# Optimization experiments

Hardware: AMD Instinct MI355X
Metric: run time of the kernel (lower is better)

The kernel has to match this reference:

```python
import jax, jax.numpy as jnp
import numpy as np

ALPHA = 0.9  # init alpha, adj='DAD'


def setup_inputs() -> dict:
    key = jax.random.key(0)
    k1, k2, k3, k4 = jax.random.split(key, 4)
    N, C, E = 100000, 64, 3200000
    labels = jax.random.uniform(k1, (N, C), dtype=jnp.float32)
    mask = jax.random.randint(k2, (N,), 0, 2).astype(bool)
    src = jax.random.randint(k3, (E,), 0, N, dtype=jnp.int64)
    dst = jax.random.randint(k4, (E,), 0, N, dtype=jnp.int64)
    return {"labels": labels, "mask": mask, "src": src, "dst": dst, "num_layers": 10}


def reference(labels, mask, src, dst, num_layers):
    N = labels.shape[0]
    # mask: y = zeros; y[mask] = labels[mask]
    y0 = jnp.where(mask[:, None], labels, jnp.zeros((), labels.dtype))
    last = (1.0 - ALPHA) * y0  # confidence = 1
    # in-degrees via scatter-count at dst, clamped to >= 1
    degs = jax.ops.segment_sum(jnp.ones(dst.shape, labels.dtype), dst, num_segments=N)
    degs = jnp.maximum(degs, 1.0)
    norm = (degs ** -0.5)[:, None]  # DAD: D^-1/2 on both sides

    def step(y, _):
        y = norm * y                                   # left D^-1/2
        h = jax.ops.segment_sum(y[src], dst, num_segments=N)  # A @ y (copy_u + sum)
        y = ALPHA * h * norm                           # right D^-1/2
        y = jnp.clip(last + y, 0.0, 1.0)               # post_step clamp
        return y, None

    y, _ = jax.lax.scan(step, y0, None, length=num_layers)
    return y
```

## Files before the change

kernel.cpp:

```cpp
#include <hip/hip_runtime.h>
#include <hip/hip_fp16.h>


#define ALPHA 0.9f
#define C 64
#define BSHIFT 7
#define MAXB 1024
#define NCHUNK 256

typedef float f32x4 __attribute__((ext_vector_type(4)));
typedef unsigned int u32;
typedef unsigned int u32x2 __attribute__((ext_vector_type(2)));


__global__ void chunk_hist_kernel(const int* __restrict__ dst, int* __restrict__ cnt,
                                  int E, int epc) {
    __shared__ int h[MAXB];
    for (int i = threadIdx.x; i < MAXB; i += 256) h[i] = 0;
    __syncthreads();
    int c = blockIdx.x;
    int e1 = min(c * epc + epc, E);
    for (int e = c * epc + threadIdx.x; e < e1; e += 256) {
        int d = __builtin_nontemporal_load(&dst[e]);
        atomicAdd(&h[d >> BSHIFT], 1);
    }
    __syncthreads();
    for (int i = threadIdx.x; i < MAXB; i += 256) cnt[i * NCHUNK + c] = h[i];
}

__global__ void chunk_scan_kernel(int* __restrict__ cnt, int* __restrict__ bucket_tot) {
    __shared__ int v[256];
    int b = blockIdx.x;
    int t = threadIdx.x;
    int x = cnt[b * NCHUNK + t];
    v[t] = x;
    __syncthreads();
    for (int off = 1; off < 256; off <<= 1) {
        int add = (t >= off) ? v[t - off] : 0;
        __syncthreads();
        v[t] += add;
        __syncthreads();
    }
    cnt[b * NCHUNK + t] = v[t] - x;
    if (t == 255) bucket_tot[b] = v[255];
}

__global__ void base_scan_kernel(const int* __restrict__ bucket_tot,
                                 int* __restrict__ bucket_base,
                                 int* __restrict__ row_ptr, int N, int E, int nb) {
    __shared__ int v[MAXB];
    int t = threadIdx.x;
    int x = (t < nb) ? bucket_tot[t] : 0;
    v[t] = x;
    __syncthreads();
    for (int off = 1; off < MAXB; off <<= 1) {
        int add = (t >= off) ? v[t - off] : 0;
        __syncthreads();
        v[t] += add;
        __syncthreads();
    }
    bucket_base[t] = v[t] - x;
    if (t == MAXB - 1) { bucket_base[MAXB] = v[MAXB - 1]; row_ptr[N] = E; }
}

__global__ void bucket_scatter_kernel(const int* __restrict__ src, const int* __restrict__ dst,
                                      const int* __restrict__ cnt,
                                      const int* __restrict__ bucket_base,
                                      unsigned* __restrict__ tmp, int E, int epc) {
    __shared__ int cur[MAXB];
    int c = blockIdx.x;
    for (int i = threadIdx.x; i < MAXB; i += 256)
        cur[i] = bucket_base[i] + cnt[i * NCHUNK + c];
    __syncthreads();
    int e1 = min(c * epc + epc, E);
    for (int e = c * epc + threadIdx.x; e < e1; e += 256) {
        int d = __builtin_nontemporal_load(&dst[e]);
        int s = __builtin_nontemporal_load(&src[e]);
        int pos = atomicAdd(&cur[d >> BSHIFT], 1);
        tmp[pos] = ((unsigned)(d & 127) << 24) | (unsigned)s;
    }
}

__global__ void bucket_sort_kernel(const unsigned* __restrict__ tmp,
                                   const int* __restrict__ bucket_base,
                                   int* __restrict__ row_ptr,
                                   float* __restrict__ norm,
                                   int* __restrict__ col, int N) {
    __shared__ int ldeg[128];
    __shared__ int lexc[128];
    __shared__ int lcur[128];
    int b = blockIdx.x;
    int lo = b << BSHIFT;
    int nn = min(128, N - lo);
    int ebeg = bucket_base[b];
    int eend = bucket_base[b + 1];
    int t = threadIdx.x;
    if (t < 128) ldeg[t] = 0;
    __syncthreads();
    for (int e = ebeg + t; e < eend; e += 256) {
        atomicAdd(&ldeg[tmp[e] >> 24], 1);
    }
    __syncthreads();
    if (t < 128) lexc[t] = ldeg[t];
    __syncthreads();
    for (int off = 1; off < 128; off <<= 1) {
        int add = (t >= off && t < 128) ? lexc[t - off] : 0;
        __syncthreads();
        if (t < 128) lexc[t] += add;
        __syncthreads();
    }
    if (t < nn) {
        int rp = ebeg + lexc[t] - ldeg[t];
        row_ptr[lo + t] = rp;
        lcur[t] = rp;
        norm[lo + t] = rsqrtf(fmaxf((float)ldeg[t], 1.0f));
    }
    __syncthreads();
    for (int e = ebeg + t; e < eend; e += 256) {
        unsigned pk = tmp[e];
        int pos = atomicAdd(&lcur[pk >> 24], 1);
        col[pos] = (int)(pk & 0xFFFFFFu);
    }
}

__global__ void pack_col_kernel(int* __restrict__ col, const float* __restrict__ norm,
                                int E) {
    int i = blockIdx.x * blockDim.x + threadIdx.x;
    if (i >= E) return;
    u32 s = (u32)col[i];
    u32 nq = (u32)(norm[s] * 32767.0f + 0.5f);
    col[i] = (int)(s | (nq << 17));
}


__global__ void init_z8_kernel(const float* __restrict__ labels,
                               const int* __restrict__ mask,
                               unsigned char* __restrict__ z8,
                               unsigned char* __restrict__ last8,
                               int total8 ) {
    int i = blockIdx.x * blockDim.x + threadIdx.x;
    if (i >= total8) return;
    int node = i >> 3;
    int g = i & 7;
    const float* lrow = labels + (size_t)node * C + g * 8;
    f32x4 a  = __builtin_nontemporal_load((const f32x4*)lrow);
    f32x4 bv = __builtin_nontemporal_load((const f32x4*)lrow + 1);
    bool mk = mask[node] != 0;
    float v[8] = {a.x, a.y, a.z, a.w, bv.x, bv.y, bv.z, bv.w};
    float m = mk ? 255.0f : 0.0f;
    u32 q0 = 0, q1 = 0;
#pragma unroll
    for (int k = 0; k < 4; ++k) q0 |= ((u32)(v[k] * m + 0.5f)) << (8 * k);
#pragma unroll
    for (int k = 0; k < 4; ++k) q1 |= ((u32)(v[k + 4] * m + 0.5f)) << (8 * k);
    u32x2 qq; qq.x = q0; qq.y = q1;
    ((u32x2*)(z8 + (size_t)node * C))[g] = qq;
    ((u32x2*)(last8 + (size_t)node * C))[g] = qq;
}


template <bool OUT_FP32>
__global__ void prop_kernel(const unsigned char* __restrict__ z8_old,
                            unsigned char* __restrict__ z8_new,
                            void* __restrict__ out_f32,
                            const int* __restrict__ row_ptr,
                            const int* __restrict__ col,
                            const float* __restrict__ norm,
                            const unsigned char* __restrict__ last8, int N) {
    int gtid = blockIdx.x * blockDim.x + threadIdx.x;
    int wid = gtid >> 6;
    int lane = threadIdx.x & 63;
    int node = (wid << 1) + (lane >> 5);
    int sub = (lane >> 3) & 3;
    int ch8 = lane & 7;

    bool ok = node < N;
    int beg = 0, end = 0;
    if (ok) { beg = row_ptr[node]; end = row_ptr[node + 1]; }
    int deg = end - beg;
    int lastc = max(end - 1, 0);
    int Tl = (deg + 3) >> 2;
    int T = max(Tl, __shfl_xor(Tl, 32, 64));

    const float DQ = 1.0f / (32767.0f * 255.0f);

    float acc[8];
#pragma unroll
    for (int k = 0; k < 8; ++k) acc[k] = 0.0f;

    if (T > 0) {
        int base = beg + sub;

        float n0, n1, n2, n3, n4, n5, n6, n7;
        uint2 r0, r1, r2, r3, r4, r5, r6, r7;

#define FETCH(t, nv, rv)                                                      \
        do {                                                                  \
            int pp = base + ((t) << 2);                                       \
            int pcl = min(pp, lastc);                                         \
            u32 pk = (u32)col[pcl];                                           \
            int sv = (int)(pk & 0x1FFFFu);                                    \
            float sc = (float)(pk >> 17) * DQ;                                \
            nv = (pp < end) ? sc : 0.0f;                                      \
            rv = ((const uint2*)(z8_old + (size_t)sv * C))[ch8];              \
        } while (0)

#define CONSUME(nv, rv)                                                       \
        do {                                                                  \
            u32 q0 = rv.x, q1 = rv.y;                                         \
            acc[0] = fmaf((float)(q0 & 0xffu),         nv, acc[0]);           \
            acc[1] = fmaf((float)((q0 >> 8) & 0xffu),  nv, acc[1]);           \
            acc[2] = fmaf((float)((q0 >> 16) & 0xffu), nv, acc[2]);           \
            acc[3] = fmaf((float)(q0 >> 24),           nv, acc[3]);           \
            acc[4] = fmaf((float)(q1 & 0xffu),         nv, acc[4]);           \
            acc[5] = fmaf((float)((q1 >> 8) & 0xffu),  nv, acc[5]);           \
            acc[6] = fmaf((float)((q1 >> 16) & 0xffu), nv, acc[6]);           \
            acc[7] = fmaf((float)(q1 >> 24),           nv, acc[7]);           \
        } while (0)

        FETCH(0, n0, r0); FETCH(1, n1, r1); FETCH(2, n2, r2); FETCH(3, n3, r3);
        FETCH(4, n4, r4); FETCH(5, n5, r5); FETCH(6, n6, r6); FETCH(7, n7, r7);
        int t = 8;
        for (; t + 8 <= T; t += 8) {
            CONSUME(n0, r0); FETCH(t + 0, n0, r0);
            CONSUME(n1, r1); FETCH(t + 1, n1, r1);
            CONSUME(n2, r2); FETCH(t + 2, n2, r2);
            CONSUME(n3, r3); FETCH(t + 3, n3, r3);
            CONSUME(n4, r4); FETCH(t + 4, n4, r4);
            CONSUME(n5, r5); FETCH(t + 5, n5, r5);
            CONSUME(n6, r6); FETCH(t + 6, n6, r6);
            CONSUME(n7, r7); FETCH(t + 7, n7, r7);
        }
        int rr = T - t;
        if (rr > 0) { CONSUME(n0, r0); FETCH(t + 0, n0, r0); }
        if (rr > 1) { CONSUME(n1, r1); FETCH(t + 1, n1, r1); }
        if (rr > 2) { CONSUME(n2, r2); FETCH(t + 2, n2, r2); }
        if (rr > 3) { CONSUME(n3, r3); FETCH(t + 3, n3, r3); }
        if (rr > 4) { CONSUME(n4, r4); FETCH(t + 4, n4, r4); }
        if (rr > 5) { CONSUME(n5, r5); FETCH(t + 5, n5, r5); }
        if (rr > 6) { CONSUME(n6, r6); FETCH(t + 6, n6, r6); }
        CONSUME(n0, r0); CONSUME(n1, r1); CONSUME(n2, r2); CONSUME(n3, r3);
        CONSUME(n4, r4); CONSUME(n5, r5); CONSUME(n6, r6); CONSUME(n7, r7);
#undef FETCH
#undef CONSUME
    }

#pragma unroll
    for (int k = 0; k < 8; ++k) {
        acc[k] += __shfl_xor(acc[k], 8, 64);
        acc[k] += __shfl_xor(acc[k], 16, 64);
    }

    if (sub == 0 && ok) {
        float nr = norm[node];
        float anr = ALPHA * nr;
        const float LC = (1.0f - ALPHA) / 255.0f;
        uint2 lq = ((const uint2*)(last8 + (size_t)node * C))[ch8];
        u32 l0 = lq.x, l1 = lq.y;
        float la[8];
        la[0] = (float)(l0 & 0xffu) * LC;
        la[1] = (float)((l0 >> 8) & 0xffu) * LC;
        la[2] = (float)((l0 >> 16) & 0xffu) * LC;
        la[3] = (float)(l0 >> 24) * LC;
        la[4] = (float)(l1 & 0xffu) * LC;
        la[5] = (float)((l1 >> 8) & 0xffu) * LC;
        la[6] = (float)((l1 >> 16) & 0xffu) * LC;
        la[7] = (float)(l1 >> 24) * LC;
        float o[8];
#pragma unroll
        for (int k = 0; k < 8; ++k)
            o[k] = fminf(fmaxf(fmaf(anr, acc[k], la[k]), 0.0f), 1.0f);
        if (OUT_FP32) {
            float* orow = (float*)out_f32 + (size_t)node * C + ch8 * 8;
            float4 v0; v0.x = o[0]; v0.y = o[1]; v0.z = o[2]; v0.w = o[3];
            float4 v1; v1.x = o[4]; v1.y = o[5]; v1.z = o[6]; v1.w = o[7];
            ((float4*)orow)[0] = v0;
            ((float4*)orow)[1] = v1;
        } else {
            u32 q0 = 0, q1 = 0;
#pragma unroll
            for (int k = 0; k < 4; ++k) q0 |= ((u32)(o[k] * 255.0f + 0.5f)) << (8 * k);
#pragma unroll
            for (int k = 0; k < 4; ++k) q1 |= ((u32)(o[k + 4] * 255.0f + 0.5f)) << (8 * k);
            uint2 qq; qq.x = q0; qq.y = q1;
            ((uint2*)(z8_new + (size_t)node * C))[ch8] = qq;
        }
    }
}


__global__ void zero_f32_kernel(float* __restrict__ p, int n) {
    int i = blockIdx.x * blockDim.x + threadIdx.x;
    if (i < n) p[i] = 0.0f;
}
__global__ void deg_count_f_kernel(const int* __restrict__ dst, float* __restrict__ deg, int E) {
    int i = blockIdx.x * blockDim.x + threadIdx.x;
    if (i < E) atomicAdd(&deg[dst[i]], 1.0f);
}
__global__ void make_norm_f_kernel(float* __restrict__ deg, int N) {
    int i = blockIdx.x * blockDim.x + threadIdx.x;
    if (i < N) deg[i] = rsqrtf(fmaxf(deg[i], 1.0f));
}
__global__ void init_yh_kernel(const float* __restrict__ labels, const int* __restrict__ mask,
                               float* __restrict__ y, float* __restrict__ h, int total4) {
    int i = blockIdx.x * blockDim.x + threadIdx.x;
    if (i >= total4) return;
    int row = i >> 4;
    float4 lv = ((const float4*)labels)[i];
    float m = (mask[row] != 0) ? 1.0f : 0.0f;
    float4 yv; yv.x = m * lv.x; yv.y = m * lv.y; yv.z = m * lv.z; yv.w = m * lv.w;
    ((float4*)y)[i] = yv;
    float4 z; z.x = 0.f; z.y = 0.f; z.z = 0.f; z.w = 0.f;
    ((float4*)h)[i] = z;
}
__global__ void scatter_kernel(const float* __restrict__ y, const int* __restrict__ src,
                               const int* __restrict__ dst, const float* __restrict__ norm,
                               float* __restrict__ h, int E) {
    int gtid = blockIdx.x * blockDim.x + threadIdx.x;
    int e = gtid >> 6;
    int lane = threadIdx.x & 63;
    if (e >= E) return;
    int s = src[e]; int d = dst[e];
    float v = y[(size_t)s * C + lane] * norm[s];
    atomicAdd(&h[(size_t)d * C + lane], v);
}
__global__ void finalize_kernel(const float* __restrict__ labels, const int* __restrict__ mask,
                                const float* __restrict__ norm, float* __restrict__ h,
                                float* __restrict__ y, int total4) {
    int i = blockIdx.x * blockDim.x + threadIdx.x;
    if (i >= total4) return;
    int row = i >> 4;
    float4 hv = ((float4*)h)[i];
    float4 lv = ((const float4*)labels)[i];
    float m = (mask[row] != 0) ? (1.0f - ALPHA) : 0.0f;
    float nr = norm[row];
    float4 o;
    o.x = fminf(fmaxf(m * lv.x + ALPHA * hv.x * nr, 0.0f), 1.0f);
    o.y = fminf(fmaxf(m * lv.y + ALPHA * hv.y * nr, 0.0f), 1.0f);
    o.z = fminf(fmaxf(m * lv.z + ALPHA * hv.z * nr, 0.0f), 1.0f);
    o.w = fminf(fmaxf(m * lv.w + ALPHA * hv.w * nr, 0.0f), 1.0f);
    ((float4*)y)[i] = o;
    float4 z; z.x = 0.f; z.y = 0.f; z.z = 0.f; z.w = 0.f;
    ((float4*)h)[i] = z;
}


extern "C" void kernel_launch(void* const* d_in, const int* in_sizes, int n_in,
                              void* d_out, int out_size, void* d_ws, size_t ws_size,
                              hipStream_t stream) {
    const float* labels = (const float*)d_in[0];
    const int*   mask   = (const int*)d_in[1];
    const int*   src    = (const int*)d_in[2];
    const int*   dst    = (const int*)d_in[3];

    const int N = in_sizes[1];
    const int E = in_sizes[2];
    const int num_layers = 10;
    const int B = 256;

    size_t fixed_ints = (size_t)(MAXB + 1) + MAXB + (size_t)NCHUNK * MAXB
                      + (N + 1) + N + E;
    size_t z8bytes = (size_t)N * C;
    size_t tmpbytes = (size_t)E * 4;
    size_t span = (tmpbytes > 2 * z8bytes ? tmpbytes : 2 * z8bytes);
    size_t need = fixed_ints * 4 + 256 + span + z8bytes;
    bool pack_ok = (N < (1 << 17));

    if (ws_size >= need && pack_ok) {
        char* w = (char*)d_ws;
        int*   bucket_base = (int*)w;             w += (size_t)(MAXB + 1) * 4;
        int*   bucket_tot  = (int*)w;             w += (size_t)MAXB * 4;
        int*   cnt         = (int*)w;             w += (size_t)NCHUNK * MAXB * 4;
        int*   row_ptr     = (int*)w;             w += (size_t)(N + 1) * 4;
        float* norm        = (float*)w;           w += (size_t)N * 4;
        int*   col         = (int*)w;             w += (size_t)E * 4;
        w = (char*)(((uintptr_t)w + 255) & ~(uintptr_t)255);
        unsigned char* z8A = (unsigned char*)w;
        unsigned char* z8B = z8A + z8bytes;
        unsigned* tmp      = (unsigned*)z8A;
        w += span;
        unsigned char* last8 = (unsigned char*)w;

        int epc = (E + NCHUNK - 1) / NCHUNK;
        int nb = (N + (1 << BSHIFT) - 1) >> BSHIFT;

        chunk_hist_kernel<<<NCHUNK, 256, 0, stream>>>(dst, cnt, E, epc);
        chunk_scan_kernel<<<nb, 256, 0, stream>>>(cnt, bucket_tot);
        base_scan_kernel<<<1, MAXB, 0, stream>>>(bucket_tot, bucket_base,
                                                 row_ptr, N, E, nb);
        bucket_scatter_kernel<<<NCHUNK, 256, 0, stream>>>(src, dst, cnt, bucket_base,
                                                          tmp, E, epc);
        bucket_sort_kernel<<<nb, 256, 0, stream>>>(tmp, bucket_base, row_ptr,
                                                   norm, col, N);
        pack_col_kernel<<<(E + B - 1) / B, B, 0, stream>>>(col, norm, E);

        int total8 = N * 8;
        init_z8_kernel<<<(total8 + B - 1) / B, B, 0, stream>>>(labels, mask,
                                                               z8A, last8, total8);
        const int nwaves = (N + 1) >> 1;
        const int prop_blocks = (int)(((size_t)nwaves * 64 + B - 1) / B);
        for (int l = 0; l < num_layers - 1; ++l) {
            unsigned char* zi = (l & 1) ? z8B : z8A;
            unsigned char* zo = (l & 1) ? z8A : z8B;
            prop_kernel<false><<<prop_blocks, B, 0, stream>>>(zi, zo, nullptr,
                                                              row_ptr, col, norm,
                                                              last8, N);
        }
        prop_kernel<true><<<prop_blocks, B, 0, stream>>>(z8B, nullptr, d_out,
                                                         row_ptr, col, norm,
                                                         last8, N);
    } else {
        const int total4 = N * C / 4;
        float* y = (float*)d_out;
        float* wsf = (float*)d_ws;
        float* norm = wsf;
        float* h = wsf + ((N + 15) & ~15);
        zero_f32_kernel<<<(N + B - 1) / B, B, 0, stream>>>(norm, N);
        deg_count_f_kernel<<<(E + B - 1) / B, B, 0, stream>>>(dst, norm, E);
        make_norm_f_kernel<<<(N + B - 1) / B, B, 0, stream>>>(norm, N);
        init_yh_kernel<<<(total4 + B - 1) / B, B, 0, stream>>>(labels, mask, y, h, total4);
        const int scatter_blocks = (int)(((size_t)E * C + B - 1) / B);
        for (int l = 0; l < num_layers; ++l) {
            scatter_kernel<<<scatter_blocks, B, 0, stream>>>(y, src, dst, norm, h, E);
            finalize_kernel<<<(total4 + B - 1) / B, B, 0, stream>>>(labels, mask, norm,
                                                                    h, y, total4);
        }
    }
}
```

Measured before the change: 650.2 us.

## Widen sort buckets and fuse norm packing into edge placement

Bucket granularity grows from 128 to 512 destination nodes, so there are fewer top-level buckets (MAXB 256). The per-bucket sort is split into a degree/row_ptr/norm kernel and a placement kernel. Because every norm value is final before placement, the placement kernel can quantise norm[src] and pack it into col directly. This removes the separate pack_col pass over all edges, at the cost of reading tmp twice and running only about 196 large 1024-thread blocks for the sort stages.

```diff
diff --git a/kernel.cpp b/kernel.cpp
--- a/kernel.cpp
+++ b/kernel.cpp
@@ -4,8 +4,8 @@
 
 #define ALPHA 0.9f
 #define C 64
-#define BSHIFT 7
-#define MAXB 1024
+#define BSHIFT 9
+#define MAXB 256
 #define NCHUNK 256
 
 typedef float f32x4 __attribute__((ext_vector_type(4)));
@@ -16,7 +16,7 @@
 __global__ void chunk_hist_kernel(const int* __restrict__ dst, int* __restrict__ cnt,
                                   int E, int epc) {
     __shared__ int h[MAXB];
-    for (int i = threadIdx.x; i < MAXB; i += 256) h[i] = 0;
+    h[threadIdx.x] = 0;
     __syncthreads();
     int c = blockIdx.x;
     int e1 = min(c * epc + epc, E);
@@ -25,7 +25,7 @@
         atomicAdd(&h[d >> BSHIFT], 1);
     }
     __syncthreads();
-    for (int i = threadIdx.x; i < MAXB; i += 256) cnt[i * NCHUNK + c] = h[i];
+    cnt[threadIdx.x * NCHUNK + c] = h[threadIdx.x];
 }
 
 __global__ void chunk_scan_kernel(int* __restrict__ cnt, int* __restrict__ bucket_tot) {
@@ -69,67 +69,68 @@
                                       unsigned* __restrict__ tmp, int E, int epc) {
     __shared__ int cur[MAXB];
     int c = blockIdx.x;
-    for (int i = threadIdx.x; i < MAXB; i += 256)
-        cur[i] = bucket_base[i] + cnt[i * NCHUNK + c];
+    cur[threadIdx.x] = bucket_base[threadIdx.x] + cnt[threadIdx.x * NCHUNK + c];
     __syncthreads();
     int e1 = min(c * epc + epc, E);
     for (int e = c * epc + threadIdx.x; e < e1; e += 256) {
         int d = __builtin_nontemporal_load(&dst[e]);
         int s = __builtin_nontemporal_load(&src[e]);
         int pos = atomicAdd(&cur[d >> BSHIFT], 1);
-        tmp[pos] = ((unsigned)(d & 127) << 24) | (unsigned)s;
-    }
-}
-
-__global__ void bucket_sort_kernel(const unsigned* __restrict__ tmp,
-                                   const int* __restrict__ bucket_base,
-                                   int* __restrict__ row_ptr,
-                                   float* __restrict__ norm,
-                                   int* __restrict__ col, int N) {
-    __shared__ int ldeg[128];
-    __shared__ int lexc[128];
-    __shared__ int lcur[128];
+        tmp[pos] = ((unsigned)(d & 511) << 23) | (unsigned)s;
+    }
+}
+
+__global__ __launch_bounds__(1024) void bucket_deg_kernel(
+        const unsigned* __restrict__ tmp, const int* __restrict__ bucket_base,
+        int* __restrict__ row_ptr, float* __restrict__ norm, int N) {
+    __shared__ int ldeg[512];
+    __shared__ int lsc[512];
     int b = blockIdx.x;
     int lo = b << BSHIFT;
-    int nn = min(128, N - lo);
+    int nn = min(512, N - lo);
     int ebeg = bucket_base[b];
     int eend = bucket_base[b + 1];
     int t = threadIdx.x;
-    if (t < 128) ldeg[t] = 0;
-    __syncthreads();
-    for (int e = ebeg + t; e < eend; e += 256) {
-        atomicAdd(&ldeg[tmp[e] >> 24], 1);
-    }
-    __syncthreads();
-    if (t < 128) lexc[t] = ldeg[t];
-    __syncthreads();
-    for (int off = 1; off < 128; off <<= 1) {
-        int add = (t >= off && t < 128) ? lexc[t - off] : 0;
-        __syncthreads();
-        if (t < 128) lexc[t] += add;
+    if (t < 512) ldeg[t] = 0;
+    __syncthreads();
+    for (int e = ebeg + t; e < eend; e += 1024) {
+        atomicAdd(&ldeg[tmp[e] >> 23], 1);
+    }
+    __syncthreads();
+    if (t < 512) lsc[t] = ldeg[t];
+    __syncthreads();
+    for (int off = 1; off < 512; off <<= 1) {
+        int add = (t >= off && t < 512) ? lsc[t - off] : 0;
+        __syncthreads();
+        if (t < 512) lsc[t] += add;
         __syncthreads();
     }
     if (t < nn) {
-        int rp = ebeg + lexc[t] - ldeg[t];
-        row_ptr[lo + t] = rp;
-        lcur[t] = rp;
+        row_ptr[lo + t] = ebeg + lsc[t] - ldeg[t];
         norm[lo + t] = rsqrtf(fmaxf((float)ldeg[t], 1.0f));
     }
-    __syncthreads();
-    for (int e = ebeg + t; e < eend; e += 256) {
+}
+
+__global__ __launch_bounds__(1024) void bucket_place_kernel(
+        const unsigned* __restrict__ tmp, const int* __restrict__ bucket_base,
+        const int* __restrict__ row_ptr, const float* __restrict__ norm,
+        int* __restrict__ col, int N) {
+    __shared__ int lcur[512];
+    int b = blockIdx.x;
+    int lo = b << BSHIFT;
+    int nn = min(512, N - lo);
+    int ebeg = bucket_base[b];
+    int eend = bucket_base[b + 1];
+    int t = threadIdx.x;
+    if (t < nn) lcur[t] = row_ptr[lo + t];
+    __syncthreads();
+    for (int e = ebeg + t; e < eend; e += 1024) {
         unsigned pk = tmp[e];
-        int pos = atomicAdd(&lcur[pk >> 24], 1);
-        col[pos] = (int)(pk & 0xFFFFFFu);
-    }
-}
-
-__global__ void pack_col_kernel(int* __restrict__ col, const float* __restrict__ norm,
-                                int E) {
-    int i = blockIdx.x * blockDim.x + threadIdx.x;
-    if (i >= E) return;
-    u32 s = (u32)col[i];
-    u32 nq = (u32)(norm[s] * 32767.0f + 0.5f);
-    col[i] = (int)(s | (nq << 17));
+        int pos = atomicAdd(&lcur[pk >> 23], 1);
+        u32 s = pk & 0x7FFFFFu;
+        u32 nq = (u32)(norm[s] * 32767.0f + 0.5f);
+        col[pos] = (int)(s | (nq << 17));
+    }
 }
 
 
@@ -390,9 +391,10 @@
                                                  row_ptr, N, E, nb);
         bucket_scatter_kernel<<<NCHUNK, 256, 0, stream>>>(src, dst, cnt, bucket_base,
                                                           tmp, E, epc);
-        bucket_sort_kernel<<<nb, 256, 0, stream>>>(tmp, bucket_base, row_ptr,
-                                                   norm, col, N);
-        pack_col_kernel<<<(E + B - 1) / B, B, 0, stream>>>(col, norm, E);
+        bucket_deg_kernel<<<nb, 1024, 0, stream>>>(tmp, bucket_base, row_ptr,
+                                                   norm, N);
+        bucket_place_kernel<<<nb, 1024, 0, stream>>>(tmp, bucket_base, row_ptr,
+                                                     norm, col, N);
 
         int total8 = N * 8;
         init_z8_kernel<<<(total8 + B - 1) / B, B, 0, stream>>>(labels, mask,
```

Result: faster. 626.7 us (-3.6%).
